# Optimization experiments

Measured on AMD Instinct MI355X. Metric: run time of the kernel, lower is better.

The kernel has to match this reference:

```python
import jax, jax.numpy as jnp
import numpy as np

B, C, U, LEN, K = 32, 16, 16, 128, 4  # batch, channels, units, image side, cheb order
POWERS = K + 1


def _path_chebyshev(n, k):
    """Chebyshev polynomials T_0..T_k of the rescaled normalized Laplacian of an
    undirected path graph with n nodes. Returns [k+1, n, n] float32."""
    A = np.zeros((n, n), dtype=np.float64)
    A[np.arange(n - 1), np.arange(1, n)] = 1.0
    A = A + A.T
    d = A.sum(axis=1)
    dinv = 1.0 / np.sqrt(d)
    L = np.eye(n) - dinv[:, None] * A * dinv[None, :]   # normalized Laplacian
    Lt = L - np.eye(n)                                   # rescaled: 2L/lambda_max - I, lambda_max=2
    T = [np.eye(n), Lt]
    for _ in range(2, k + 1):
        T.append(2.0 * Lt @ T[-1] - T[-2])
    return np.stack(T[: k + 1]).astype(np.float32)


def setup_inputs() -> dict:
    key = jax.random.key(0)
    kx, kc = jax.random.split(key)
    x = jax.random.normal(kx, (B, C, LEN, LEN), dtype=jnp.float32)
    coefs = 0.001 * jax.random.normal(kc, (POWERS, POWERS, C, U), dtype=jnp.float32)
    cheb = jnp.asarray(_path_chebyshev(LEN, K))  # same graph for both axes
    return {"x": x, "coefs": coefs, "cheb1": cheb, "cheb2": cheb}


def reference(x, coefs, cheb1, cheb2):
    # out[b,u,p,q] = sum_{k1,k2,c,h,w} coefs[k1,k2,c,u] * cheb1[k1,h,p] * x[b,c,h,w] * cheb2[k2,w,q]
    t1 = jnp.einsum('bchw,khp->bkcpw', x, cheb1)        # apply cheb1 along H
    s = jnp.einsum('bkcpw,klcu->blupw', t1, coefs)      # contract k1 and channels
    out = jnp.einsum('blupw,lwq->bupq', s, cheb2)       # apply cheb2 along W, contract k2
    return out
```

## Files before the change

kernel.cpp:

```cpp
#include <hip/hip_runtime.h>
#include <hip/hip_bf16.h>

#define LEN 128
#define NB 32
#define NC 16
#define NU 16
#define NK 5
#define KC 80
#define KCP 96

typedef unsigned int uint32;
typedef unsigned short ushort16;
typedef __attribute__((ext_vector_type(8))) short bf16x8;
typedef __attribute__((ext_vector_type(4))) float f32x4;

#define MFMA(a, b, c) __builtin_amdgcn_mfma_f32_16x16x32_bf16(a, b, c, 0, 0, 0)

#define SIG(r) (((r) & 15) ^ (((r) >> 3) & 15))

static __device__ inline ushort16 f2bf(float f) {
    union { float f; uint32 u; } v; v.f = f;
    uint32 u = v.u;
    uint32 r = (u + 0x7fffu + ((u >> 16) & 1u)) >> 16;
    return (ushort16)r;
}
static __device__ inline uint32 pkbf(float a, float b) {
    return (uint32)f2bf(a) | ((uint32)f2bf(b) << 16);
}
static __device__ inline bf16x8 frag16(const void* p) {
    return *(const bf16x8*)p;
}

__global__ __launch_bounds__(256) void kprep(const float* __restrict__ x,
                                             const float* __restrict__ coefs,
                                             const float* __restrict__ cheb1,
                                             const float* __restrict__ cheb2,
                                             ushort16* __restrict__ xF,
                                             ushort16* __restrict__ cheb1F,
                                             ushort16* __restrict__ cheb2F,
                                             ushort16* __restrict__ coefF) {
    __shared__ __align__(16) uint32 Xs[128 * 64];
    const int blk = blockIdx.x, tid = threadIdx.x;
    if (blk < 512) {
        const int bc = blk;
        const float* xp = x + (size_t)bc * (LEN * LEN);
        {
            int w = tid & 127, hg = tid >> 7;
            #pragma unroll
            for (int uu = 0; uu < 8; ++uu) {
                int u = hg * 8 + uu;
                uint4 d;
                uint32* dp = (uint32*)&d;
                #pragma unroll
                for (int t = 0; t < 4; ++t) {
                    int h2 = u * 4 + t;
                    dp[t] = pkbf(xp[(2 * h2) * LEN + w], xp[(2 * h2 + 1) * LEN + w]);
                }
                *(uint4*)(Xs + w * 64 + ((u ^ SIG(w)) << 2)) = d;
            }
        }
        __syncthreads();
        ushort16* dst = xF + (size_t)bc * 16384;
        #pragma unroll
        for (int i = 0; i < 8; ++i) {
            int n = tid + i * 256;
            int lane = n & 63, fk = n >> 6;
            int wrow = (fk >> 2) * 16 + (lane & 15);
            int u = (fk & 3) * 4 + (lane >> 4);
            uint4 v = *(const uint4*)(Xs + wrow * 64 + ((u ^ SIG(wrow)) << 2));
            *(uint4*)(dst + (size_t)n * 8) = v;
        }
    } else {
        int i = (blk - 512) * 256 + tid;
        if (i < 81920) {
            int j = i & 7, lane = (i >> 3) & 63, ks = (i >> 9) & 3, nt = i >> 11;
            int kp = nt * 16 + (lane & 15);
            int k = kp >> 7, p = kp & 127;
            int h = ks * 32 + ((lane >> 4) << 3) + j;
            cheb1F[i] = f2bf(cheb1[(k * LEN + h) * LEN + p]);
        } else if (i < 163840) {
            int i2 = i - 81920;
            int j = i2 & 7, lane = (i2 >> 3) & 63, t = i2 >> 9;
            int ks = t % 20, nt = t / 20;
            int q = nt * 16 + (lane & 15);
            int lw = ks * 32 + ((lane >> 4) << 3) + j;
            int l = lw >> 7, w = lw & 127;
            cheb2F[i2] = f2bf(cheb2[(l * LEN + w) * LEN + q]);
        } else {
            int i3 = i - 163840;
            int j = i3 & 7, lane = (i3 >> 3) & 63, t = i3 >> 9;
            int ks = t % 3, nt = t / 3;
            int lu = nt * 16 + (lane & 15);
            int l = lu >> 4, u = lu & 15;
            int kc = ks * 32 + ((lane >> 4) << 3) + j;
            int k = kc >> 4, c = kc & 15;
            coefF[i3] = (kc < KC) ? f2bf(coefs[((k * NK + l) * NC + c) * NU + u]) : (ushort16)0;
        }
    }
}

__global__ __launch_bounds__(256, 5) void k1_mfma(const ushort16* __restrict__ xF,
                                                  const ushort16* __restrict__ cheb1F,
                                                  ushort16* __restrict__ t1, int b0) {
    __shared__ __align__(16) uint32 Bs[64 * 64];
    const int c = blockIdx.x, bl = blockIdx.y, z = blockIdx.z;
    const int b = b0 + bl;
    const int tid = threadIdx.x;
    const int lane = tid & 63, wm = tid >> 6;
    const int m16 = lane & 15, g = lane >> 4;

    const ushort16* xFb = xF + ((size_t)(b * NC + c)) * 16384;

    f32x4 acc[2][4];
    #pragma unroll
    for (int mi = 0; mi < 2; ++mi)
        #pragma unroll
        for (int ni = 0; ni < 4; ++ni) acc[mi][ni] = (f32x4)0.f;

    #pragma unroll
    for (int ks = 0; ks < 4; ++ks) {
        bf16x8 Af[2], Bf[4];
        #pragma unroll
        for (int mi = 0; mi < 2; ++mi) {
            int mt = wm * 2 + mi;
            Af[mi] = frag16(xFb + ((size_t)(mt * 4 + ks) * 64 + lane) * 8);
        }
        #pragma unroll
        for (int ni = 0; ni < 4; ++ni) {
            int nt = 8 + z * 4 + ni;
            Bf[ni] = frag16(cheb1F + ((size_t)(nt * 4 + ks) * 64 + lane) * 8);
        }
        #pragma unroll
        for (int mi = 0; mi < 2; ++mi)
            #pragma unroll
            for (int ni = 0; ni < 4; ++ni)
                acc[mi][ni] = MFMA(Af[mi], Bf[ni], acc[mi][ni]);
    }

    #pragma unroll
    for (int ni = 0; ni < 4; ++ni)
        #pragma unroll
        for (int mi = 0; mi < 2; ++mi) {
            int rr = ni * 16 + m16;
            int wu = wm * 32 + mi * 16 + g * 4;
            uint2 d;
            d.x = pkbf(acc[mi][ni][0], acc[mi][ni][1]);
            d.y = pkbf(acc[mi][ni][2], acc[mi][ni][3]);
            int u = wu >> 3;
            *(uint2*)(Bs + rr * 64 + ((u ^ SIG(rr)) << 2) + ((wu >> 1) & 3)) = d;
        }
    __syncthreads();

    #pragma unroll
    for (int i = 0; i < 4; ++i) {
        int n = tid + i * 256;
        int rr = n >> 4, wsg = n & 15;
        uint4 v = *(const uint4*)(Bs + rr * 64 + ((wsg ^ SIG(rr)) << 2));
        int kp = 128 + z * 64 + rr;
        int k = kp >> 7, p = kp & 127;
        *(uint4*)(t1 + ((size_t)((bl * LEN + p) * KC + k * NC + c)) * LEN + wsg * 8) = v;
    }
}

__global__ __launch_bounds__(256, 5) void k2_mfma(const ushort16* __restrict__ t1,
                                                  const float* __restrict__ x,
                                                  const ushort16* __restrict__ coefF,
                                                  const ushort16* __restrict__ cheb2F,
                                                  float* __restrict__ out, int b0) {
    __shared__ __align__(16) uint32 sm[128 * 64];
    const int p = blockIdx.x, bl = blockIdx.y, b = b0 + bl;
    const int tid = threadIdx.x;
    const int lane = tid & 63, wave = tid >> 6;
    const int n16 = lane & 15, g = lane >> 4;

    const uint32* t1u = (const uint32*)(t1 + (size_t)(bl * LEN + p) * (KC * LEN));
    uint4 Av[2], Bv[2];
    #pragma unroll
    for (int i = 0; i < 2; ++i) {
        int it = tid + i * 256;
        int a2 = 8 + (it >> 4), wq = it & 15;
        const uint32* src = t1u + a2 * 128 + wq * 4;
        Av[i] = *(const uint4*)(src);
        Bv[i] = *(const uint4*)(src + 64);
    }
    float4 X0, X1;
    {
        int j = tid >> 5, w0 = (tid & 31) << 2;
        const float* xb = x + ((size_t)(b * NC) * LEN + p) * LEN;
        const float* xa = xb + (size_t)(2 * j) * (LEN * LEN);
        X0 = *(const float4*)(xa + w0);
        X1 = *(const float4*)(xa + LEN * LEN + w0);
    }
    #pragma unroll
    for (int i = 0; i < 4; ++i) {
        int idx = tid + i * 256;
        int row = idx >> 3, d = idx & 7;
        int u = 10 + (d >> 2);
        sm[row * 64 + ((u ^ SIG(row)) << 2) + (d & 3)] = 0;
    }
    {
        int j = tid >> 5, w0 = (tid & 31) << 2;
        const float* f0 = (const float*)&X0;
        const float* f1 = (const float*)&X1;
        int u0 = j >> 2, lo = j & 3;
        #pragma unroll
        for (int r = 0; r < 4; ++r) {
            int row = w0 + r;
            sm[row * 64 + ((u0 ^ SIG(row)) << 2) + lo] = pkbf(f0[r], f1[r]);
        }
    }
    #pragma unroll
    for (int i = 0; i < 2; ++i) {
        int it = tid + i * 256;
        int a2 = 8 + (it >> 4), wq = it & 15;
        const uint32* av = (const uint32*)&Av[i];
        const uint32* bv = (const uint32*)&Bv[i];
        int u = a2 >> 2, lo = a2 & 3;
        #pragma unroll
        for (int j = 0; j < 4; ++j) {
            int r0 = wq * 8 + 2 * j, r1 = r0 + 1;
            sm[r0 * 64 + ((u ^ SIG(r0)) << 2) + lo] = (av[j] & 0xffffu) | (bv[j] << 16);
            sm[r1 * 64 + ((u ^ SIG(r1)) << 2) + lo] = (av[j] >> 16) | (bv[j] & 0xffff0000u);
        }
    }
    __syncthreads();

    f32x4 acc[2][5];
    #pragma unroll
    for (int mi = 0; mi < 2; ++mi)
        #pragma unroll
        for (int ni = 0; ni < 5; ++ni) acc[mi][ni] = (f32x4)0.f;

    #pragma unroll
    for (int ks = 0; ks < 3; ++ks) {
        bf16x8 Af[2], Bf[5];
        #pragma unroll
        for (int mi = 0; mi < 2; ++mi) {
            int row = wave * 32 + mi * 16 + n16;
            Af[mi] = frag16(sm + row * 64 + (((ks * 4 + g) ^ SIG(row)) << 2));
        }
        #pragma unroll
        for (int ni = 0; ni < 5; ++ni)
            Bf[ni] = frag16(coefF + ((size_t)(ni * 3 + ks) * 64 + lane) * 8);
        #pragma unroll
        for (int mi = 0; mi < 2; ++mi)
            #pragma unroll
            for (int ni = 0; ni < 5; ++ni)
                acc[mi][ni] = MFMA(Af[mi], Bf[ni], acc[mi][ni]);
    }
    __syncthreads();

    {
        ushort16* A3 = (ushort16*)sm;
        #pragma unroll
        for (int mi = 0; mi < 2; ++mi)
            #pragma unroll
            for (int ni = 0; ni < 5; ++ni) {
                int wcol = wave * 32 + mi * 16 + g * 4;
                uint2 d;
                d.x = pkbf(acc[mi][ni][0], acc[mi][ni][1]);
                d.y = pkbf(acc[mi][ni][2], acc[mi][ni][3]);
                *(uint2*)(A3 + n16 * 648 + ni * 128 + wcol) = d;
            }
    }
    __syncthreads();

    const ushort16* A3r = (const ushort16*)sm;
    f32x4 c3[2];
    c3[0] = (f32x4)0.f; c3[1] = (f32x4)0.f;
    #pragma unroll 4
    for (int ks = 4; ks < 20; ++ks) {
        bf16x8 Aa = frag16(A3r + n16 * 648 + ks * 32 + g * 8);
        #pragma unroll
        for (int nt = 0; nt < 2; ++nt) {
            bf16x8 Bb = frag16(cheb2F + ((size_t)((wave * 2 + nt) * 20 + ks) * 64 + lane) * 8);
            c3[nt] = MFMA(Aa, Bb, c3[nt]);
        }
    }

    #pragma unroll
    for (int nt = 0; nt < 2; ++nt)
        #pragma unroll
        for (int r = 0; r < 4; ++r) {
            int u = g * 4 + r;
            int q = wave * 32 + nt * 16 + n16;
            uint32 bf = ((uint32)A3r[u * 648 + q]) << 16;
            float l0 = __uint_as_float(bf);
            out[(((size_t)(b * NU + u)) * LEN + p) * LEN + q] = c3[nt][r] + l0;
        }
}

extern "C" void kernel_launch(void* const* d_in, const int* in_sizes, int n_in,
                              void* d_out, int out_size, void* d_ws, size_t ws_size,
                              hipStream_t stream) {
    const float* x     = (const float*)d_in[0];
    const float* coefs = (const float*)d_in[1];
    const float* cheb1 = (const float*)d_in[2];
    const float* cheb2 = (const float*)d_in[3];
    float* out = (float*)d_out;

    const size_t xF_bytes  = (size_t)NB * NC * 16384 * sizeof(ushort16);
    const size_t aux_bytes = 163840 + 163840 + 15360;
    size_t off = (ws_size - aux_bytes - xF_bytes) & ~(size_t)255;
    ushort16* cheb1F = (ushort16*)((char*)d_ws + off);
    ushort16* cheb2F = cheb1F + 81920;
    ushort16* coefF  = cheb2F + 81920;
    ushort16* xF     = coefF + 7680;
    ushort16* t1 = (ushort16*)d_ws;

    const size_t per_b = (size_t)LEN * KC * LEN * sizeof(ushort16);
    int chunk = (int)(off / per_b);
    if (chunk < 1) chunk = 1;
    if (chunk > NB) chunk = NB;

    hipLaunchKernelGGL(kprep, dim3(1182), dim3(256), 0, stream,
                       x, coefs, cheb1, cheb2, xF, cheb1F, cheb2F, coefF);
    for (int b0 = 0; b0 < NB; b0 += chunk) {
        int cb = (NB - b0 < chunk) ? (NB - b0) : chunk;
        hipLaunchKernelGGL(k1_mfma, dim3(NC, cb, 8), dim3(256), 0, stream,
                           xF, cheb1F, t1, b0);
        hipLaunchKernelGGL(k2_mfma, dim3(LEN, cb), dim3(256), 0, stream,
                           t1, x, coefF, cheb2F, out, b0);
    }
}
```

Measured before the change: 149.5 us.

## Fuse x bf16 conversion into the cheb1 MFMA kernel, dropping the xF buffer

The x-to-bf16 transpose formerly written to a global xF buffer is now staged only in shared memory inside the first-stage kernel. That block then loops over all 8 output slabs instead of using a z grid dimension. This removes an 8 MB global write and read of xF and one kernel's worth of x traffic. In exchange the first-stage grid shrinks eightfold to NC*cb blocks with more work per block, and the launch bound drops to 3 blocks per SM, which reduces parallelism and latency hiding.

```diff
diff --git a/kernel.cpp b/kernel.cpp
--- a/kernel.cpp
+++ b/kernel.cpp
@@ -31,134 +31,119 @@
     return *(const bf16x8*)p;
 }
 
-__global__ __launch_bounds__(256) void kprep(const float* __restrict__ x,
-                                             const float* __restrict__ coefs,
-                                             const float* __restrict__ cheb1,
-                                             const float* __restrict__ cheb2,
-                                             ushort16* __restrict__ xF,
-                                             ushort16* __restrict__ cheb1F,
-                                             ushort16* __restrict__ cheb2F,
-                                             ushort16* __restrict__ coefF) {
+__global__ __launch_bounds__(256) void kconst(const float* __restrict__ coefs,
+                                              const float* __restrict__ cheb1,
+                                              const float* __restrict__ cheb2,
+                                              ushort16* __restrict__ cheb1F,
+                                              ushort16* __restrict__ cheb2F,
+                                              ushort16* __restrict__ coefF) {
+    int i = blockIdx.x * 256 + threadIdx.x;
+    if (i < 81920) {
+        int j = i & 7, lane = (i >> 3) & 63, ks = (i >> 9) & 3, nt = i >> 11;
+        int kp = nt * 16 + (lane & 15);
+        int k = kp >> 7, p = kp & 127;
+        int h = ks * 32 + ((lane >> 4) << 3) + j;
+        cheb1F[i] = f2bf(cheb1[(k * LEN + h) * LEN + p]);
+    } else if (i < 163840) {
+        int i2 = i - 81920;
+        int j = i2 & 7, lane = (i2 >> 3) & 63, t = i2 >> 9;
+        int ks = t % 20, nt = t / 20;
+        int q = nt * 16 + (lane & 15);
+        int lw = ks * 32 + ((lane >> 4) << 3) + j;
+        int l = lw >> 7, w = lw & 127;
+        cheb2F[i2] = f2bf(cheb2[(l * LEN + w) * LEN + q]);
+    } else {
+        int i3 = i - 163840;
+        int j = i3 & 7, lane = (i3 >> 3) & 63, t = i3 >> 9;
+        int ks = t % 3, nt = t / 3;
+        int lu = nt * 16 + (lane & 15);
+        int l = lu >> 4, u = lu & 15;
+        int kc = ks * 32 + ((lane >> 4) << 3) + j;
+        int k = kc >> 4, c = kc & 15;
+        coefF[i3] = (kc < KC) ? f2bf(coefs[((k * NK + l) * NC + c) * NU + u]) : (ushort16)0;
+    }
+}
+
+__global__ __launch_bounds__(256, 3) void kfuse(const float* __restrict__ x,
+                                                const ushort16* __restrict__ cheb1F,
+                                                ushort16* __restrict__ t1, int b0) {
     __shared__ __align__(16) uint32 Xs[128 * 64];
-    const int blk = blockIdx.x, tid = threadIdx.x;
-    if (blk < 512) {
-        const int bc = blk;
-        const float* xp = x + (size_t)bc * (LEN * LEN);
-        {
-            int w = tid & 127, hg = tid >> 7;
-            #pragma unroll
-            for (int uu = 0; uu < 8; ++uu) {
-                int u = hg * 8 + uu;
-                uint4 d;
-                uint32* dp = (uint32*)&d;
-                #pragma unroll
-                for (int t = 0; t < 4; ++t) {
-                    int h2 = u * 4 + t;
-                    dp[t] = pkbf(xp[(2 * h2) * LEN + w], xp[(2 * h2 + 1) * LEN + w]);
-                }
-                *(uint4*)(Xs + w * 64 + ((u ^ SIG(w)) << 2)) = d;
-            }
-        }
-        __syncthreads();
-        ushort16* dst = xF + (size_t)bc * 16384;
-        #pragma unroll
-        for (int i = 0; i < 8; ++i) {
-            int n = tid + i * 256;
-            int lane = n & 63, fk = n >> 6;
-            int wrow = (fk >> 2) * 16 + (lane & 15);
-            int u = (fk & 3) * 4 + (lane >> 4);
-            uint4 v = *(const uint4*)(Xs + wrow * 64 + ((u ^ SIG(wrow)) << 2));
-            *(uint4*)(dst + (size_t)n * 8) = v;
-        }
-    } else {
-        int i = (blk - 512) * 256 + tid;
-        if (i < 81920) {
-            int j = i & 7, lane = (i >> 3) & 63, ks = (i >> 9) & 3, nt = i >> 11;
-            int kp = nt * 16 + (lane & 15);
-            int k = kp >> 7, p = kp & 127;
-            int h = ks * 32 + ((lane >> 4) << 3) + j;
-            cheb1F[i] = f2bf(cheb1[(k * LEN + h) * LEN + p]);
-        } else if (i < 163840) {
-            int i2 = i - 81920;
-            int j = i2 & 7, lane = (i2 >> 3) & 63, t = i2 >> 9;
-            int ks = t % 20, nt = t / 20;
-            int q = nt * 16 + (lane & 15);
-            int lw = ks * 32 + ((lane >> 4) << 3) + j;
-            int l = lw >> 7, w = lw & 127;
-            cheb2F[i2] = f2bf(cheb2[(l * LEN + w) * LEN + q]);
-        } else {
-            int i3 = i - 163840;
-            int j = i3 & 7, lane = (i3 >> 3) & 63, t = i3 >> 9;
-            int ks = t % 3, nt = t / 3;
-            int lu = nt * 16 + (lane & 15);
-            int l = lu >> 4, u = lu & 15;
-            int kc = ks * 32 + ((lane >> 4) << 3) + j;
-            int k = kc >> 4, c = kc & 15;
-            coefF[i3] = (kc < KC) ? f2bf(coefs[((k * NK + l) * NC + c) * NU + u]) : (ushort16)0;
-        }
-    }
-}
-
-__global__ __launch_bounds__(256, 5) void k1_mfma(const ushort16* __restrict__ xF,
-                                                  const ushort16* __restrict__ cheb1F,
-                                                  ushort16* __restrict__ t1, int b0) {
     __shared__ __align__(16) uint32 Bs[64 * 64];
-    const int c = blockIdx.x, bl = blockIdx.y, z = blockIdx.z;
-    const int b = b0 + bl;
+    const int c = blockIdx.x, bl = blockIdx.y, b = b0 + bl;
     const int tid = threadIdx.x;
     const int lane = tid & 63, wm = tid >> 6;
     const int m16 = lane & 15, g = lane >> 4;
 
-    const ushort16* xFb = xF + ((size_t)(b * NC + c)) * 16384;
-
-    f32x4 acc[2][4];
-    #pragma unroll
-    for (int mi = 0; mi < 2; ++mi)
-        #pragma unroll
-        for (int ni = 0; ni < 4; ++ni) acc[mi][ni] = (f32x4)0.f;
-
-    #pragma unroll
-    for (int ks = 0; ks < 4; ++ks) {
-        bf16x8 Af[2], Bf[4];
-        #pragma unroll
-        for (int mi = 0; mi < 2; ++mi) {
-            int mt = wm * 2 + mi;
-            Af[mi] = frag16(xFb + ((size_t)(mt * 4 + ks) * 64 + lane) * 8);
-        }
-        #pragma unroll
-        for (int ni = 0; ni < 4; ++ni) {
-            int nt = 8 + z * 4 + ni;
-            Bf[ni] = frag16(cheb1F + ((size_t)(nt * 4 + ks) * 64 + lane) * 8);
-        }
+    {
+        const float* xp = x + (size_t)(b * NC + c) * (LEN * LEN);
+        int w = tid & 127, hg = tid >> 7;
+        #pragma unroll
+        for (int uu = 0; uu < 8; ++uu) {
+            int u = hg * 8 + uu;
+            uint4 d;
+            uint32* dp = (uint32*)&d;
+            #pragma unroll
+            for (int t = 0; t < 4; ++t) {
+                int h2 = u * 4 + t;
+                dp[t] = pkbf(xp[(2 * h2) * LEN + w], xp[(2 * h2 + 1) * LEN + w]);
+            }
+            *(uint4*)(Xs + w * 64 + ((u ^ SIG(w)) << 2)) = d;
+        }
+    }
+    __syncthreads();
+
+    for (int ns = 0; ns < 8; ++ns) {
+        f32x4 acc[2][4];
         #pragma unroll
         for (int mi = 0; mi < 2; ++mi)
             #pragma unroll
-            for (int ni = 0; ni < 4; ++ni)
-                acc[mi][ni] = MFMA(Af[mi], Bf[ni], acc[mi][ni]);
-    }
-
-    #pragma unroll
-    for (int ni = 0; ni < 4; ++ni)
-        #pragma unroll
-        for (int mi = 0; mi < 2; ++mi) {
-            int rr = ni * 16 + m16;
-            int wu = wm * 32 + mi * 16 + g * 4;
-            uint2 d;
-            d.x = pkbf(acc[mi][ni][0], acc[mi][ni][1]);
-            d.y = pkbf(acc[mi][ni][2], acc[mi][ni][3]);
-            int u = wu >> 3;
-            *(uint2*)(Bs + rr * 64 + ((u ^ SIG(rr)) << 2) + ((wu >> 1) & 3)) = d;
-        }
-    __syncthreads();
-
-    #pragma unroll
-    for (int i = 0; i < 4; ++i) {
-        int n = tid + i * 256;
-        int rr = n >> 4, wsg = n & 15;
-        uint4 v = *(const uint4*)(Bs + rr * 64 + ((wsg ^ SIG(rr)) << 2));
-        int kp = 128 + z * 64 + rr;
-        int k = kp >> 7, p = kp & 127;
-        *(uint4*)(t1 + ((size_t)((bl * LEN + p) * KC + k * NC + c)) * LEN + wsg * 8) = v;
+            for (int ni = 0; ni < 4; ++ni) acc[mi][ni] = (f32x4)0.f;
+
+        #pragma unroll
+        for (int ks = 0; ks < 4; ++ks) {
+            bf16x8 Af[2], Bf[4];
+            #pragma unroll
+            for (int mi = 0; mi < 2; ++mi) {
+                int wrow = (wm * 2 + mi) * 16 + m16;
+                Af[mi] = frag16(Xs + wrow * 64 + (((ks * 4 + g) ^ SIG(wrow)) << 2));
+            }
+            #pragma unroll
+            for (int ni = 0; ni < 4; ++ni) {
+                int nt = 8 + ns * 4 + ni;
+                Bf[ni] = frag16(cheb1F + ((size_t)(nt * 4 + ks) * 64 + lane) * 8);
+            }
+            #pragma unroll
+            for (int mi = 0; mi < 2; ++mi)
+                #pragma unroll
+                for (int ni = 0; ni < 4; ++ni)
+                    acc[mi][ni] = MFMA(Af[mi], Bf[ni], acc[mi][ni]);
+        }
+
+        if (ns) __syncthreads();
+
+        #pragma unroll
+        for (int ni = 0; ni < 4; ++ni)
+            #pragma unroll
+            for (int mi = 0; mi < 2; ++mi) {
+                int rr = ni * 16 + m16;
+                int wu = wm * 32 + mi * 16 + g * 4;
+                uint2 d;
+                d.x = pkbf(acc[mi][ni][0], acc[mi][ni][1]);
+                d.y = pkbf(acc[mi][ni][2], acc[mi][ni][3]);
+                int u = wu >> 3;
+                *(uint2*)(Bs + rr * 64 + ((u ^ SIG(rr)) << 2) + ((wu >> 1) & 3)) = d;
+            }
+        __syncthreads();
+
+        #pragma unroll
+        for (int i = 0; i < 4; ++i) {
+            int n = tid + i * 256;
+            int rr = n >> 4, wsg = n & 15;
+            uint4 v = *(const uint4*)(Bs + rr * 64 + ((wsg ^ SIG(rr)) << 2));
+            int kp = 128 + ns * 64 + rr;
+            int k = kp >> 7, p = kp & 127;
+            *(uint4*)(t1 + ((size_t)((bl * LEN + p) * KC + k * NC + c)) * LEN + wsg * 8) = v;
+        }
     }
 }
 
@@ -299,13 +284,11 @@
     const float* cheb2 = (const float*)d_in[3];
     float* out = (float*)d_out;
 
-    const size_t xF_bytes  = (size_t)NB * NC * 16384 * sizeof(ushort16);
     const size_t aux_bytes = 163840 + 163840 + 15360;
-    size_t off = (ws_size - aux_bytes - xF_bytes) & ~(size_t)255;
+    size_t off = (ws_size - aux_bytes) & ~(size_t)255;
     ushort16* cheb1F = (ushort16*)((char*)d_ws + off);
     ushort16* cheb2F = cheb1F + 81920;
     ushort16* coefF  = cheb2F + 81920;
-    ushort16* xF     = coefF + 7680;
     ushort16* t1 = (ushort16*)d_ws;
 
     const size_t per_b = (size_t)LEN * KC * LEN * sizeof(ushort16);
@@ -313,12 +296,12 @@
     if (chunk < 1) chunk = 1;
     if (chunk > NB) chunk = NB;
 
-    hipLaunchKernelGGL(kprep, dim3(1182), dim3(256), 0, stream,
-                       x, coefs, cheb1, cheb2, xF, cheb1F, cheb2F, coefF);
+    hipLaunchKernelGGL(kconst, dim3(670), dim3(256), 0, stream,
+                       coefs, cheb1, cheb2, cheb1F, cheb2F, coefF);
     for (int b0 = 0; b0 < NB; b0 += chunk) {
         int cb = (NB - b0 < chunk) ? (NB - b0) : chunk;
-        hipLaunchKernelGGL(k1_mfma, dim3(NC, cb, 8), dim3(256), 0, stream,
-                           xF, cheb1F, t1, b0);
+        hipLaunchKernelGGL(kfuse, dim3(NC, cb), dim3(256), 0, stream,
+                           x, cheb1F, t1, b0);
         hipLaunchKernelGGL(k2_mfma, dim3(LEN, cb), dim3(256), 0, stream,
                            t1, x, coefF, cheb2F, out, b0);
     }
```

Measured after the change: 148.7 us. Within noise of the previous version (-0.5%).
